# Optimization experiments

Measured on AMD Instinct MI355X. Metric: run time of the kernel, lower is better.

The kernel has to match this reference:

```python
import jax, jax.numpy as jnp
import numpy as np

D_MODEL = 256
N_LAYERS = 8
NUM_CLASSES = 3
INPUT_DIM = 1
BATCH = 8
SEQ = 2048
EXIT_IDX = (1, 3, 5, 7)  # n_layers//4-1, n_layers//2-1, 3n//4-1, n-1
LN_EPS = 1e-5


def setup_inputs() -> dict:
    key = jax.random.key(0)
    ks = jax.random.split(key, 16)
    d, nl, nc = D_MODEL, N_LAYERS, NUM_CLASSES
    return {
        "x": jax.random.normal(ks[0], (BATCH, SEQ, INPUT_DIM), jnp.float32),
        "in_W": jax.random.normal(ks[1], (d, INPUT_DIM), jnp.float32) * 0.02,
        "in_b": jnp.zeros((d,), jnp.float32),
        "A_params": jax.random.normal(ks[2], (nl, d), jnp.float32) * 0.1,
        "B_params": jax.random.normal(ks[3], (nl, d), jnp.float32),
        "C_params": jax.random.normal(ks[4], (nl, d), jnp.float32),
        "D_params": jax.random.normal(ks[5], (nl, d), jnp.float32),
        "proj_W": jax.random.normal(ks[6], (nl, d, d), jnp.float32) * 0.02,
        "proj_b": jnp.zeros((nl, d), jnp.float32),
        "ln_g": jnp.ones((nl, d), jnp.float32),
        "ln_b": jnp.zeros((nl, d), jnp.float32),
        "head_W": jax.random.normal(ks[7], (4, nc, d), jnp.float32) * 0.02,
        "head_b": jnp.zeros((4, nc), jnp.float32),
    }


def _ssm_block(x, Ap, Bp, Cp, Dp, pW, pb, g, b):
    # x: [B, L, d]
    Bsz, L, d = x.shape
    A = jax.nn.sigmoid(Ap)                               # [d]
    t = jnp.arange(L, dtype=jnp.float32)
    K = (Cp[:, None] * (A[:, None] ** t[None, :]) * Bp[:, None])[:, None, :]  # [d,1,L]
    xt = jnp.swapaxes(x, 1, 2)                           # [B, d, L]
    # torch F.conv1d(pad=L-1, groups=d) then [..., :L] == left-pad-only cross-correlation
    out = jax.lax.conv_general_dilated(
        xt, K, window_strides=(1,), padding=[(L - 1, 0)], feature_group_count=d
    )                                                    # [B, d, L]
    out = out + Dp[None, :, None] * xt
    out = jnp.swapaxes(out, 1, 2)                        # [B, L, d]
    out = jax.nn.gelu(out, approximate=False) @ pW.T + pb
    y = x + out
    mu = jnp.mean(y, axis=-1, keepdims=True)
    var = jnp.var(y, axis=-1, keepdims=True)
    return (y - mu) / jnp.sqrt(var + LN_EPS) * g + b


def reference(x, in_W, in_b, A_params, B_params, C_params, D_params,
              proj_W, proj_b, ln_g, ln_b, head_W, head_b):
    h = x @ in_W.T + in_b                                # [B, L, d]
    logits = []
    head = 0
    for i in range(N_LAYERS):
        h = _ssm_block(h, A_params[i], B_params[i], C_params[i], D_params[i],
                       proj_W[i], proj_b[i], ln_g[i], ln_b[i])
        if i in EXIT_IDX:
            pooled = jnp.mean(h, axis=1)                 # [B, d]
            logits.append(pooled @ head_W[head].T + head_b[head])
            head += 1
    return jnp.stack(logits, axis=0)                     # [4, B, num_classes]
```

## Files before the change

kernel.cpp:

```cpp
#include <hip/hip_runtime.h>
#include <math.h>

#define DM 256
#define LSEQ 2048
#define BATCH 8
#define NLAYER 8
#define EMAX 192
#define LN_EPS 1e-5f
#define BM 64
#define ROWS (BATCH * LSEQ)

#define HT_STRIDE 1040
#define AB_OFF   66560
#define AL_OFF   (AB_OFF + 32768)
#define RED_OFF  (AL_OFF + 32768)
#define SMEM_SZ  (RED_OFF + 2048)

typedef float f32x4 __attribute__((ext_vector_type(4)));
typedef short bf16x8 __attribute__((ext_vector_type(8)));
typedef unsigned short u16;
typedef unsigned short u16x4 __attribute__((ext_vector_type(4)));
typedef unsigned short u16x8 __attribute__((ext_vector_type(8)));

union V8 { u16x8 u; bf16x8 b; };

__device__ __forceinline__ float gelu_exact(float v) {
    return 0.5f * v * (1.f + erff(v * 0.70710678118654752f));
}

__device__ __forceinline__ void split2(float g, u16& hi, u16& lo) {
    unsigned u = __float_as_uint(g);
    hi = (u16)(u >> 16);
    float fh = __uint_as_float(u & 0xFFFF0000u);
    float r = g - fh;
    unsigned v = __float_as_uint(r);
    v = v + 0x7FFFu + ((v >> 16) & 1u);
    lo = (u16)(v >> 16);
}

__global__ void k_prepW(const float* __restrict__ pW, u16* __restrict__ pWh,
                        u16* __restrict__ pWl) {
    int i = blockIdx.x * blockDim.x + threadIdx.x;
    int e = i * 8;
    int l = e >> 16;
    int r = e & 65535;
    int cg = r >> 12;
    int ks = (r >> 9) & 7;
    int lane = (r >> 3) & 63;
    int fq = lane >> 4, fr = lane & 15;
    int col = (cg >> 2) * 64 + (cg & 3) * 16 + fr;
    int k = ks * 32 + fq * 8;
    const float* src = pW + l * 65536 + col * 256 + k;
    float4 w0 = *(const float4*)src;
    float4 w1 = *(const float4*)(src + 4);
    float vv[8] = {w0.x, w0.y, w0.z, w0.w, w1.x, w1.y, w1.z, w1.w};
    u16 sh[8], sl[8];
#pragma unroll
    for (int j = 0; j < 8; ++j) split2(vv[j], sh[j], sl[j]);
    u16x8 vh = {sh[0], sh[1], sh[2], sh[3], sh[4], sh[5], sh[6], sh[7]};
    u16x8 vl = {sl[0], sl[1], sl[2], sl[3], sl[4], sl[5], sl[6], sl[7]};
    *(u16x8*)&pWh[e] = vh;
    *(u16x8*)&pWl[e] = vl;
}

__global__ void k_prep0(const float* __restrict__ x, const float* __restrict__ inW,
                        const float* __restrict__ inb, const float* __restrict__ Ap,
                        const float* __restrict__ Bp, const float* __restrict__ Cp,
                        float* __restrict__ P_all, float* __restrict__ logA_all,
                        float* __restrict__ CB_all, float* __restrict__ pooled,
                        int* __restrict__ flags) {
    int b = blockIdx.x;
    int c = threadIdx.x;
    float A0 = 1.f / (1.f + expf(-Ap[c]));
    float iw = inW[c], ib = inb[c];
    const float* xb = x + b * LSEQ;
    float pw = 1.f, acc = 0.f;
    for (int t = 0; t <= EMAX; ++t) {
        acc += (xb[t] * iw + ib) * pw;
        pw *= A0;
    }
    P_all[b * DM + c] = acc;
    for (int l = 1; l < NLAYER; ++l) P_all[l * BATCH * DM + b * DM + c] = 0.f;
    for (int e = 0; e < 4; ++e) pooled[e * BATCH * DM + b * DM + c] = 0.f;
    if (b == 0) {
        for (int l = 0; l < NLAYER; ++l) {
            float Al = 1.f / (1.f + expf(-Ap[l * DM + c]));
            logA_all[l * DM + c] = logf(Al);
            CB_all[l * DM + c]   = Bp[l * DM + c] * Cp[l * DM + c];
        }
        if (c < NLAYER * BATCH) flags[c] = 0;
    }
}

__global__ __launch_bounds__(512, 2) void k_fused(
    const float* __restrict__ x, const float* __restrict__ inW,
    const float* __restrict__ inb,
    const u16* __restrict__ pWh, const u16* __restrict__ pWl,
    const float* __restrict__ Dp_all, const float* __restrict__ pb_all,
    const float* __restrict__ lng_all, const float* __restrict__ lnb_all,
    const float* __restrict__ logA_all, const float* __restrict__ CB_all,
    float* __restrict__ P_all, float* __restrict__ pooled,
    int* __restrict__ flags)
{
    __shared__ __align__(16) char smem[SMEM_SZ];

    int tid  = threadIdx.x;
    int lane = tid & 63;
    int wv   = tid >> 6;
    int wm   = wv >> 2;
    int wn   = wv & 3;
    int fr   = lane & 15;
    int fq   = lane >> 4;

    int b    = blockIdx.x >> 5;
    int blk  = blockIdx.x & 31;
    int brow = b * LSEQ + blk * BM;
    bool isTail = (blk >= 28);
    bool isProd = (blk <= 3);

    int srow = tid >> 3;
    int gr_s = brow + srow;
    int t_s  = gr_s & (LSEQ - 1);
    int u_s  = (LSEQ - 1) - t_s;
    bool tail_s = (u_s <= EMAX);
    float uf = (float)u_s;
    float xv = x[gr_s];

    float hreg[2][4][4];
    float* Pbuf = (float*)(smem + RED_OFF);

    for (int l = 0; l < NLAYER; ++l) {
        const float* Dp  = Dp_all   + l * DM;
        const float* la  = logA_all + l * DM;
        const float* cbp = CB_all   + l * DM;

        if (isTail) {
            if (l >= 1 && tid == 0) {
                while (__hip_atomic_load(&flags[l * BATCH + b], __ATOMIC_ACQUIRE,
                                         __HIP_MEMORY_SCOPE_AGENT) < 4)
                    __builtin_amdgcn_s_sleep(2);
            }
            __syncthreads();
            if (tid < DM)
                Pbuf[tid] = __hip_atomic_load(
                    &P_all[(size_t)l * BATCH * DM + b * DM + tid],
                    __ATOMIC_RELAXED, __HIP_MEMORY_SCOPE_AGENT);
            __syncthreads();
        }

#pragma unroll
        for (int i = 0; i < 4; ++i) {
            int u  = (tid & 7) + 8 * i;
            int kk = u * 8;
            int hby = srow * HT_STRIDE + u * 32;
            float hv[8];
            if (l == 0) {
                float4 w0 = *(const float4*)&inW[kk], w1 = *(const float4*)&inW[kk + 4];
                float4 b0 = *(const float4*)&inb[kk], b1 = *(const float4*)&inb[kk + 4];
                hv[0] = fmaf(xv, w0.x, b0.x); hv[1] = fmaf(xv, w0.y, b0.y);
                hv[2] = fmaf(xv, w0.z, b0.z); hv[3] = fmaf(xv, w0.w, b0.w);
                hv[4] = fmaf(xv, w1.x, b1.x); hv[5] = fmaf(xv, w1.y, b1.y);
                hv[6] = fmaf(xv, w1.z, b1.z); hv[7] = fmaf(xv, w1.w, b1.w);
                float4 o0 = {hv[0], hv[1], hv[2], hv[3]};
                float4 o1 = {hv[4], hv[5], hv[6], hv[7]};
                *(float4*)(smem + hby) = o0;
                *(float4*)(smem + hby + 16) = o1;
            } else {
                float4 h0 = *(const float4*)(smem + hby);
                float4 h1 = *(const float4*)(smem + hby + 16);
                hv[0] = h0.x; hv[1] = h0.y; hv[2] = h0.z; hv[3] = h0.w;
                hv[4] = h1.x; hv[5] = h1.y; hv[6] = h1.z; hv[7] = h1.w;
            }
            float4 d0 = *(const float4*)&Dp[kk];
            float4 d1 = *(const float4*)&Dp[kk + 4];
            float vv[8];
            vv[0] = hv[0] * d0.x; vv[1] = hv[1] * d0.y;
            vv[2] = hv[2] * d0.z; vv[3] = hv[3] * d0.w;
            vv[4] = hv[4] * d1.x; vv[5] = hv[5] * d1.y;
            vv[6] = hv[6] * d1.z; vv[7] = hv[7] * d1.w;
            if (tail_s) {
                float4 la0 = *(const float4*)&la[kk],  la1 = *(const float4*)&la[kk + 4];
                float4 cb0 = *(const float4*)&cbp[kk], cb1 = *(const float4*)&cbp[kk + 4];
                float4 P0  = *(const float4*)&Pbuf[kk], P1 = *(const float4*)&Pbuf[kk + 4];
                vv[0] += cb0.x * expf(uf * la0.x) * P0.x;
                vv[1] += cb0.y * expf(uf * la0.y) * P0.y;
                vv[2] += cb0.z * expf(uf * la0.z) * P0.z;
                vv[3] += cb0.w * expf(uf * la0.w) * P0.w;
                vv[4] += cb1.x * expf(uf * la1.x) * P1.x;
                vv[5] += cb1.y * expf(uf * la1.y) * P1.y;
                vv[6] += cb1.z * expf(uf * la1.z) * P1.z;
                vv[7] += cb1.w * expf(uf * la1.w) * P1.w;
            }
            u16 sh[8], sl[8];
#pragma unroll
            for (int j = 0; j < 8; ++j) split2(gelu_exact(vv[j]), sh[j], sl[j]);
            u16x8 vh = {sh[0], sh[1], sh[2], sh[3], sh[4], sh[5], sh[6], sh[7]};
            u16x8 vl = {sl[0], sl[1], sl[2], sl[3], sl[4], sl[5], sl[6], sl[7]};
            int aby = srow * 512 + ((u ^ (srow & 7)) << 4);
            *(u16x8*)(smem + AB_OFF + aby) = vh;
            *(u16x8*)(smem + AL_OFF + aby) = vl;
        }
        __syncthreads();

        f32x4 acc[2][4];
#pragma unroll
        for (int m = 0; m < 2; ++m)
#pragma unroll
            for (int n = 0; n < 4; ++n) acc[m][n] = (f32x4){0.f, 0.f, 0.f, 0.f};

        const u16* bhp = pWh + (size_t)l * 65536 + wn * 16384 + lane * 8;
        const u16* blp = pWl + (size_t)l * 65536 + wn * 16384 + lane * 8;

        V8 bhd[2][4], bld[2][4];
#pragma unroll
        for (int n = 0; n < 4; ++n) {
            bhd[0][n].u = *(const u16x8*)&bhp[n * 4096];
            bld[0][n].u = *(const u16x8*)&blp[n * 4096];
        }
#pragma unroll
        for (int ks = 0; ks < 8; ++ks) {
            int cur = ks & 1, nxt = cur ^ 1;
            if (ks < 7) {
#pragma unroll
                for (int n = 0; n < 4; ++n) {
                    bhd[nxt][n].u = *(const u16x8*)&bhp[n * 4096 + (ks + 1) * 512];
                    bld[nxt][n].u = *(const u16x8*)&blp[n * 4096 + (ks + 1) * 512];
                }
            }
            V8 ah[2], al[2];
#pragma unroll
            for (int m = 0; m < 2; ++m) {
                int row = wm * 32 + m * 16 + fr;
                int aby = row * 512 + (((ks * 4 + fq) ^ (row & 7)) << 4);
                ah[m].u = *(const u16x8*)(smem + AB_OFF + aby);
                al[m].u = *(const u16x8*)(smem + AL_OFF + aby);
            }
#pragma unroll
            for (int m = 0; m < 2; ++m)
#pragma unroll
                for (int n = 0; n < 4; ++n) {
                    acc[m][n] = __builtin_amdgcn_mfma_f32_16x16x32_bf16(ah[m].b, bhd[cur][n].b, acc[m][n], 0, 0, 0);
                    acc[m][n] = __builtin_amdgcn_mfma_f32_16x16x32_bf16(ah[m].b, bld[cur][n].b, acc[m][n], 0, 0, 0);
                    acc[m][n] = __builtin_amdgcn_mfma_f32_16x16x32_bf16(al[m].b, bhd[cur][n].b, acc[m][n], 0, 0, 0);
                }
        }

        if (l == 0) {
#pragma unroll
            for (int m = 0; m < 2; ++m)
#pragma unroll
                for (int n = 0; n < 4; ++n)
#pragma unroll
                    for (int r = 0; r < 4; ++r) {
                        int row = wm * 32 + m * 16 + fq * 4 + r;
                        int col = wn * 64 + n * 16 + fr;
                        hreg[m][n][r] = *(const float*)(smem + row * HT_STRIDE + col * 4);
                    }
        }
        float pbv[4], lgv[4], lbv[4];
#pragma unroll
        for (int n = 0; n < 4; ++n) {
            int col = wn * 64 + n * 16 + fr;
            pbv[n] = pb_all[l * DM + col];
            lgv[n] = lng_all[l * DM + col];
            lbv[n] = lnb_all[l * DM + col];
        }
        float s[2][4], ss[2][4];
#pragma unroll
        for (int m = 0; m < 2; ++m)
#pragma unroll
            for (int r = 0; r < 4; ++r) {
                float sy = 0.f, sy2 = 0.f;
#pragma unroll
                for (int n = 0; n < 4; ++n) {
                    float y = hreg[m][n][r] + acc[m][n][r] + pbv[n];
                    acc[m][n][r] = y;
                    sy += y; sy2 += y * y;
                }
                s[m][r] = sy; ss[m][r] = sy2;
            }
#pragma unroll
        for (int m = 0; m < 2; ++m)
#pragma unroll
            for (int r = 0; r < 4; ++r)
#pragma unroll
                for (int msk = 1; msk < 16; msk <<= 1) {
                    s[m][r]  += __shfl_xor(s[m][r],  msk);
                    ss[m][r] += __shfl_xor(ss[m][r], msk);
                }
        if (fr == 0) {
#pragma unroll
            for (int m = 0; m < 2; ++m)
#pragma unroll
                for (int r = 0; r < 4; ++r) {
                    int row = wm * 32 + m * 16 + fq * 4 + r;
                    *(float*)(smem + RED_OFF + (row * 8 + wn * 2)     * 4) = s[m][r];
                    *(float*)(smem + RED_OFF + (row * 8 + wn * 2 + 1) * 4) = ss[m][r];
                }
        }
        __syncthreads();

        float mean[2][4], rstd[2][4];
#pragma unroll
        for (int m = 0; m < 2; ++m)
#pragma unroll
            for (int r = 0; r < 4; ++r) {
                int row = wm * 32 + m * 16 + fq * 4 + r;
                float st = 0.f, sst = 0.f;
#pragma unroll
                for (int w = 0; w < 4; ++w) {
                    st  += *(const float*)(smem + RED_OFF + (row * 8 + w * 2)     * 4);
                    sst += *(const float*)(smem + RED_OFF + (row * 8 + w * 2 + 1) * 4);
                }
                float mu = st * (1.f / 256.f);
                float var = sst * (1.f / 256.f) - mu * mu;
                mean[m][r] = mu;
                rstd[m][r] = rsqrtf(var + LN_EPS);
            }
        int slot = (l == 1) ? 0 : (l == 3) ? 1 : (l == 5) ? 2 : (l == 7) ? 3 : -1;
        bool prod = (l < NLAYER - 1) && isProd;
        float lanv[4];
        if (prod) {
            const float* lan = logA_all + (l + 1) * DM;
#pragma unroll
            for (int n = 0; n < 4; ++n) lanv[n] = lan[wn * 64 + n * 16 + fr];
        }
        float cs[4] = {0.f, 0.f, 0.f, 0.f};
        float pc[4] = {0.f, 0.f, 0.f, 0.f};
#pragma unroll
        for (int m = 0; m < 2; ++m)
#pragma unroll
            for (int r = 0; r < 4; ++r) {
                int row  = wm * 32 + m * 16 + fq * 4 + r;
                int trow = blk * BM + row;
#pragma unroll
                for (int n = 0; n < 4; ++n) {
                    float o = (acc[m][n][r] - mean[m][r]) * rstd[m][r] * lgv[n] + lbv[n];
                    hreg[m][n][r] = o;
                    int col = wn * 64 + n * 16 + fr;
                    *(float*)(smem + row * HT_STRIDE + col * 4) = o;
                    if (slot >= 0) cs[n] += o;
                    if (prod && trow <= EMAX) pc[n] += o * expf((float)trow * lanv[n]);
                }
            }
        if (slot >= 0) {
#pragma unroll
            for (int n = 0; n < 4; ++n) {
                cs[n] += __shfl_xor(cs[n], 16);
                cs[n] += __shfl_xor(cs[n], 32);
            }
            if (lane < 16) {
#pragma unroll
                for (int n = 0; n < 4; ++n)
                    atomicAdd(&pooled[slot * (BATCH * DM) + b * DM + wn * 64 + n * 16 + lane], cs[n]);
            }
        }
        if (prod) {
#pragma unroll
            for (int n = 0; n < 4; ++n) {
                pc[n] += __shfl_xor(pc[n], 16);
                pc[n] += __shfl_xor(pc[n], 32);
            }
            if (lane < 16) {
#pragma unroll
                for (int n = 0; n < 4; ++n)
                    atomicAdd(&P_all[(size_t)(l + 1) * BATCH * DM + b * DM + wn * 64 + n * 16 + lane], pc[n]);
            }
        }
        __syncthreads();
        if (prod && tid == 0)
            __hip_atomic_fetch_add(&flags[(l + 1) * BATCH + b], 1,
                                   __ATOMIC_RELEASE, __HIP_MEMORY_SCOPE_AGENT);
    }
}

__global__ void k_head(const float* __restrict__ pooled, const float* __restrict__ hW,
                       const float* __restrict__ hb, float* __restrict__ out) {
    int tid = threadIdx.x;
    if (tid >= 96) return;
    int e = tid / 24;
    int r = tid % 24;
    int b = r / 3;
    int n = r % 3;
    const float* pv = &pooled[e * (BATCH * DM) + b * DM];
    const float* wv = &hW[(e * 3 + n) * DM];
    float acc = 0.f;
    for (int c = 0; c < DM; ++c) acc += pv[c] * wv[c];
    out[e * 24 + b * 3 + n] = acc * (1.f / (float)LSEQ) + hb[e * 3 + n];
}

extern "C" void kernel_launch(void* const* d_in, const int* in_sizes, int n_in,
                              void* d_out, int out_size, void* d_ws, size_t ws_size,
                              hipStream_t stream) {
    const float* x   = (const float*)d_in[0];
    const float* inW = (const float*)d_in[1];
    const float* inb = (const float*)d_in[2];
    const float* Ap  = (const float*)d_in[3];
    const float* Bp  = (const float*)d_in[4];
    const float* Cp  = (const float*)d_in[5];
    const float* Dp  = (const float*)d_in[6];
    const float* pW  = (const float*)d_in[7];
    const float* pb  = (const float*)d_in[8];
    const float* lng = (const float*)d_in[9];
    const float* lnb = (const float*)d_in[10];
    const float* hW  = (const float*)d_in[11];
    const float* hb  = (const float*)d_in[12];
    float* out = (float*)d_out;

    float* ws = (float*)d_ws;
    float* P_all    = ws;
    float* logA_all = P_all + NLAYER * BATCH * DM;
    float* CB_all   = logA_all + NLAYER * DM;
    float* pooled   = CB_all + NLAYER * DM;
    u16* pWh        = (u16*)(pooled + 4 * BATCH * DM);
    u16* pWl        = pWh + NLAYER * DM * DM;
    int* flags      = (int*)(pWl + NLAYER * DM * DM);

    k_prepW<<<(NLAYER * DM * DM / 8) / 256, 256, 0, stream>>>(pW, pWh, pWl);
    k_prep0<<<BATCH, 256, 0, stream>>>(x, inW, inb, Ap, Bp, Cp,
                                       P_all, logA_all, CB_all, pooled, flags);
    k_fused<<<BATCH * 32, 512, 0, stream>>>(
        x, inW, inb, pWh, pWl, Dp, pb, lng, lnb,
        logA_all, CB_all, P_all, pooled, flags);
    k_head<<<1, 128, 0, stream>>>(pooled, hW, hb, out);
}
```

Before: 135.9 us.

## Halve row tile to 32 rows, double block count, use fast erf/exp approximations

Shrinks each block to 32 rows and 256 threads (4 waves split over N), launching 64 blocks per batch (512 total) instead of 256 blocks. Producer and tail block counts are retuned, with 7 producer blocks covering the first EMAX rows and tails from block 57. The weight-fragment prefetch is hoisted above the GELU/A-tile build so it overlaps that work. Exact erff/expf are replaced by an Abramowitz-Stegun erf polynomial and __expf, which cuts transcendental cost at some loss of accuracy. Each block still streams the full layer weights, so global weight traffic per row roughly doubles, and more blocks spin-wait on the producer flags.

```diff
diff --git a/kernel.cpp b/kernel.cpp
--- a/kernel.cpp
+++ b/kernel.cpp
@@ -7,14 +7,17 @@
 #define NLAYER 8
 #define EMAX 192
 #define LN_EPS 1e-5f
-#define BM 64
+#define BM 32
+#define BLKS 64
+#define NPROD 7
+#define TAILB 57
 #define ROWS (BATCH * LSEQ)
 
 #define HT_STRIDE 1040
-#define AB_OFF   66560
-#define AL_OFF   (AB_OFF + 32768)
-#define RED_OFF  (AL_OFF + 32768)
-#define SMEM_SZ  (RED_OFF + 2048)
+#define AB_OFF   33280
+#define AL_OFF   (AB_OFF + 16384)
+#define RED_OFF  (AL_OFF + 16384)
+#define SMEM_SZ  (RED_OFF + 1280)
 
 typedef float f32x4 __attribute__((ext_vector_type(4)));
 typedef short bf16x8 __attribute__((ext_vector_type(8)));
@@ -24,8 +27,21 @@
 
 union V8 { u16x8 u; bf16x8 b; };
 
-__device__ __forceinline__ float gelu_exact(float v) {
-    return 0.5f * v * (1.f + erff(v * 0.70710678118654752f));
+__device__ __forceinline__ float erf_fast(float x) {
+    float ax = fabsf(x);
+    float t = __builtin_amdgcn_rcpf(fmaf(0.3275911f, ax, 1.f));
+    float p = fmaf(t, 1.061405429f, -1.453152027f);
+    p = fmaf(t, p, 1.421413741f);
+    p = fmaf(t, p, -0.284496736f);
+    p = fmaf(t, p, 0.254829592f);
+    p = p * t;
+    float e = __expf(-ax * ax);
+    float r = 1.f - p * e;
+    return copysignf(r, x);
+}
+
+__device__ __forceinline__ float gelu_fast(float v) {
+    return 0.5f * v * (1.f + erf_fast(v * 0.70710678118654752f));
 }
 
 __device__ __forceinline__ void split2(float g, u16& hi, u16& lo) {
@@ -92,7 +108,7 @@
     }
 }
 
-__global__ __launch_bounds__(512, 2) void k_fused(
+__global__ __launch_bounds__(256, 2) void k_fused(
     const float* __restrict__ x, const float* __restrict__ inW,
     const float* __restrict__ inb,
     const u16* __restrict__ pWh, const u16* __restrict__ pWl,
@@ -106,17 +122,15 @@
 
     int tid  = threadIdx.x;
     int lane = tid & 63;
-    int wv   = tid >> 6;
-    int wm   = wv >> 2;
-    int wn   = wv & 3;
+    int wn   = tid >> 6;
     int fr   = lane & 15;
     int fq   = lane >> 4;
 
-    int b    = blockIdx.x >> 5;
-    int blk  = blockIdx.x & 31;
+    int b    = blockIdx.x >> 6;
+    int blk  = blockIdx.x & 63;
     int brow = b * LSEQ + blk * BM;
-    bool isTail = (blk >= 28);
-    bool isProd = (blk <= 3);
+    bool isTail = (blk >= TAILB);
+    bool isProd = (blk < NPROD);
 
     int srow = tid >> 3;
     int gr_s = brow + srow;
@@ -137,7 +151,7 @@
         if (isTail) {
             if (l >= 1 && tid == 0) {
                 while (__hip_atomic_load(&flags[l * BATCH + b], __ATOMIC_ACQUIRE,
-                                         __HIP_MEMORY_SCOPE_AGENT) < 4)
+                                         __HIP_MEMORY_SCOPE_AGENT) < NPROD)
                     __builtin_amdgcn_s_sleep(2);
             }
             __syncthreads();
@@ -146,6 +160,15 @@
                     &P_all[(size_t)l * BATCH * DM + b * DM + tid],
                     __ATOMIC_RELAXED, __HIP_MEMORY_SCOPE_AGENT);
             __syncthreads();
+        }
+
+        const u16* bhp = pWh + (size_t)l * 65536 + wn * 16384 + lane * 8;
+        const u16* blp = pWl + (size_t)l * 65536 + wn * 16384 + lane * 8;
+        V8 bhd[2][4], bld[2][4];
+#pragma unroll
+        for (int n = 0; n < 4; ++n) {
+            bhd[0][n].u = *(const u16x8*)&bhp[n * 4096];
+            bld[0][n].u = *(const u16x8*)&blp[n * 4096];
         }
 
 #pragma unroll
@@ -182,18 +205,18 @@
                 float4 la0 = *(const float4*)&la[kk],  la1 = *(const float4*)&la[kk + 4];
                 float4 cb0 = *(const float4*)&cbp[kk], cb1 = *(const float4*)&cbp[kk + 4];
                 float4 P0  = *(const float4*)&Pbuf[kk], P1 = *(const float4*)&Pbuf[kk + 4];
-                vv[0] += cb0.x * expf(uf * la0.x) * P0.x;
-                vv[1] += cb0.y * expf(uf * la0.y) * P0.y;
-                vv[2] += cb0.z * expf(uf * la0.z) * P0.z;
-                vv[3] += cb0.w * expf(uf * la0.w) * P0.w;
-                vv[4] += cb1.x * expf(uf * la1.x) * P1.x;
-                vv[5] += cb1.y * expf(uf * la1.y) * P1.y;
-                vv[6] += cb1.z * expf(uf * la1.z) * P1.z;
-                vv[7] += cb1.w * expf(uf * la1.w) * P1.w;
+                vv[0] += cb0.x * __expf(uf * la0.x) * P0.x;
+                vv[1] += cb0.y * __expf(uf * la0.y) * P0.y;
+                vv[2] += cb0.z * __expf(uf * la0.z) * P0.z;
+                vv[3] += cb0.w * __expf(uf * la0.w) * P0.w;
+                vv[4] += cb1.x * __expf(uf * la1.x) * P1.x;
+                vv[5] += cb1.y * __expf(uf * la1.y) * P1.y;
+                vv[6] += cb1.z * __expf(uf * la1.z) * P1.z;
+                vv[7] += cb1.w * __expf(uf * la1.w) * P1.w;
             }
             u16 sh[8], sl[8];
 #pragma unroll
-            for (int j = 0; j < 8; ++j) split2(gelu_exact(vv[j]), sh[j], sl[j]);
+            for (int j = 0; j < 8; ++j) split2(gelu_fast(vv[j]), sh[j], sl[j]);
             u16x8 vh = {sh[0], sh[1], sh[2], sh[3], sh[4], sh[5], sh[6], sh[7]};
             u16x8 vl = {sl[0], sl[1], sl[2], sl[3], sl[4], sl[5], sl[6], sl[7]};
             int aby = srow * 512 + ((u ^ (srow & 7)) << 4);
@@ -208,15 +231,6 @@
 #pragma unroll
             for (int n = 0; n < 4; ++n) acc[m][n] = (f32x4){0.f, 0.f, 0.f, 0.f};
 
-        const u16* bhp = pWh + (size_t)l * 65536 + wn * 16384 + lane * 8;
-        const u16* blp = pWl + (size_t)l * 65536 + wn * 16384 + lane * 8;
-
-        V8 bhd[2][4], bld[2][4];
-#pragma unroll
-        for (int n = 0; n < 4; ++n) {
-            bhd[0][n].u = *(const u16x8*)&bhp[n * 4096];
-            bld[0][n].u = *(const u16x8*)&blp[n * 4096];
-        }
 #pragma unroll
         for (int ks = 0; ks < 8; ++ks) {
             int cur = ks & 1, nxt = cur ^ 1;
@@ -230,7 +244,7 @@
             V8 ah[2], al[2];
 #pragma unroll
             for (int m = 0; m < 2; ++m) {
-                int row = wm * 32 + m * 16 + fr;
+                int row = m * 16 + fr;
                 int aby = row * 512 + (((ks * 4 + fq) ^ (row & 7)) << 4);
                 ah[m].u = *(const u16x8*)(smem + AB_OFF + aby);
                 al[m].u = *(const u16x8*)(smem + AL_OFF + aby);
@@ -252,7 +266,7 @@
                 for (int n = 0; n < 4; ++n)
 #pragma unroll
                     for (int r = 0; r < 4; ++r) {
-                        int row = wm * 32 + m * 16 + fq * 4 + r;
+                        int row = m * 16 + fq * 4 + r;
                         int col = wn * 64 + n * 16 + fr;
                         hreg[m][n][r] = *(const float*)(smem + row * HT_STRIDE + col * 4);
                     }
@@ -293,9 +307,9 @@
             for (int m = 0; m < 2; ++m)
 #pragma unroll
                 for (int r = 0; r < 4; ++r) {
-                    int row = wm * 32 + m * 16 + fq * 4 + r;
-                    *(float*)(smem + RED_OFF + (row * 8 + wn * 2)     * 4) = s[m][r];
-                    *(float*)(smem + RED_OFF + (row * 8 + wn * 2 + 1) * 4) = ss[m][r];
+                    int row = m * 16 + fq * 4 + r;
+                    *(float*)(smem + RED_OFF + (row * 10 + wn * 2)     * 4) = s[m][r];
+                    *(float*)(smem + RED_OFF + (row * 10 + wn * 2 + 1) * 4) = ss[m][r];
                 }
         }
         __syncthreads();
@@ -305,12 +319,12 @@
         for (int m = 0; m < 2; ++m)
 #pragma unroll
             for (int r = 0; r < 4; ++r) {
-                int row = wm * 32 + m * 16 + fq * 4 + r;
+                int row = m * 16 + fq * 4 + r;
                 float st = 0.f, sst = 0.f;
 #pragma unroll
                 for (int w = 0; w < 4; ++w) {
-                    st  += *(const float*)(smem + RED_OFF + (row * 8 + w * 2)     * 4);
-                    sst += *(const float*)(smem + RED_OFF + (row * 8 + w * 2 + 1) * 4);
+                    st  += *(const float*)(smem + RED_OFF + (row * 10 + w * 2)     * 4);
+                    sst += *(const float*)(smem + RED_OFF + (row * 10 + w * 2 + 1) * 4);
                 }
                 float mu = st * (1.f / 256.f);
                 float var = sst * (1.f / 256.f) - mu * mu;
@@ -331,7 +345,7 @@
         for (int m = 0; m < 2; ++m)
 #pragma unroll
             for (int r = 0; r < 4; ++r) {
-                int row  = wm * 32 + m * 16 + fq * 4 + r;
+                int row  = m * 16 + fq * 4 + r;
                 int trow = blk * BM + row;
 #pragma unroll
                 for (int n = 0; n < 4; ++n) {
@@ -340,7 +354,7 @@
                     int col = wn * 64 + n * 16 + fr;
                     *(float*)(smem + row * HT_STRIDE + col * 4) = o;
                     if (slot >= 0) cs[n] += o;
-                    if (prod && trow <= EMAX) pc[n] += o * expf((float)trow * lanv[n]);
+                    if (prod && trow <= EMAX) pc[n] += o * __expf((float)trow * lanv[n]);
                 }
             }
         if (slot >= 0) {
@@ -419,7 +433,7 @@
     k_prepW<<<(NLAYER * DM * DM / 8) / 256, 256, 0, stream>>>(pW, pWh, pWl);
     k_prep0<<<BATCH, 256, 0, stream>>>(x, inW, inb, Ap, Bp, Cp,
                                        P_all, logA_all, CB_all, pooled, flags);
-    k_fused<<<BATCH * 32, 512, 0, stream>>>(
+    k_fused<<<BATCH * BLKS, 256, 0, stream>>>(
         x, inW, inb, pWh, pWl, Dp, pb, lng, lnb,
         logA_all, CB_all, P_all, pooled, flags);
     k_head<<<1, 128, 0, stream>>>(pooled, hW, hb, out);
```

New measurement: 121.7 us. 1.12x faster.
